# Optimization experiments

Hardware: AMD Instinct MI355X
Metric: run time of the kernel (lower is better)

The kernel has to match this reference:

```python
import jax, jax.numpy as jnp
import numpy as np

# Mamba2 hyperparameters
D_MODEL = 768
D_STATE = 64
D_CONV = 4
EXPAND = 2
HEADDIM = 64
CHUNK = 64
D_INNER = EXPAND * D_MODEL            # 1536
NHEADS = D_INNER // HEADDIM           # 24
D_IN_PROJ = 2 * D_INNER + 2 * D_STATE + NHEADS  # 3224
CONV_DIM = D_INNER + 2 * D_STATE      # 1664
B_SZ = 8
SEQ = 4096  # multiple of CHUNK -> no padding branch


def setup_inputs() -> dict:
    key = jax.random.key(0)
    ks = jax.random.split(key, 6)
    u = jax.random.normal(ks[0], (B_SZ, SEQ, D_MODEL), jnp.float32)
    # fan-in scaled weights (matches nn.Linear/Conv1d default init scale)
    W_in = jax.random.normal(ks[1], (D_IN_PROJ, D_MODEL), jnp.float32) / np.sqrt(D_MODEL).astype(np.float32)
    conv_w = jax.random.normal(ks[2], (CONV_DIM, 1, D_CONV), jnp.float32) / np.sqrt(D_CONV).astype(np.float32)
    conv_b = jnp.zeros((CONV_DIM,), jnp.float32)
    dt_bias = jax.random.uniform(ks[3], (NHEADS,), jnp.float32, -4.0, 1.0)  # nn.init.uniform_(-4, 1)
    A_log = jnp.full((NHEADS,), -np.log(2.0), jnp.float32)                  # nn.init.constant_(-log 2)
    D_param = jnp.ones((NHEADS,), jnp.float32)
    norm_w = jnp.ones((D_INNER,), jnp.float32)
    W_out = jax.random.normal(ks[4], (D_MODEL, D_INNER), jnp.float32) / np.sqrt(D_INNER).astype(np.float32)
    return dict(u=u, W_in=W_in, conv_w=conv_w, conv_b=conv_b, dt_bias=dt_bias,
                A_log=A_log, D_param=D_param, norm_w=norm_w, W_out=W_out)


def _segsum(x):
    """Stable segment sum: out[..., i, j] = sum_{j < k <= i} x[..., k]; -inf above diagonal."""
    T = x.shape[-1]
    lower_strict = jnp.tril(jnp.ones((T, T), bool), -1)
    xe = jnp.where(lower_strict, x[..., :, None], 0.0)   # broadcast x over last (col) axis
    s = jnp.cumsum(xe, axis=-2)
    lower = jnp.tril(jnp.ones((T, T), bool), 0)
    return jnp.where(lower, s, -jnp.inf)


def _ssd(x, A, B, C, chunk):
    """Chunked SSD. x:(b,L,h,p)  A:(b,L,h)  B,C:(b,L,1,n)."""
    b, L, h, p = x.shape
    c = L // chunk
    n = B.shape[-1]
    x = x.reshape(b, c, chunk, h, p)
    A = A.reshape(b, c, chunk, h).transpose(0, 3, 1, 2)   # b h c l
    B = B.reshape(b, c, chunk, 1, n)
    C = C.reshape(b, c, chunk, 1, n)
    A_cs = jnp.cumsum(A, axis=-1)                          # b h c l
    # intra-chunk (diagonal) term
    Lmat = jnp.exp(_segsum(A))                             # b h c l s
    Y_diag = jnp.einsum('bclhn,bcshn,bhcls,bcshp->bclhp', C, B, Lmat, x)
    # per-chunk states
    decay_states = jnp.exp(A_cs[..., -1:] - A_cs)          # b h c l
    states = jnp.einsum('bclhn,bhcl,bclhp->bchpn', B, decay_states, x)
    states = jnp.concatenate([jnp.zeros_like(states[:, :1]), states], axis=1)  # b (c+1) h p n
    # inter-chunk recurrence
    A_last = jnp.pad(A_cs[..., -1], ((0, 0), (0, 0), (1, 0)))  # b h (c+1)
    decay_chunk = jnp.exp(_segsum(A_last))                     # b h (c+1) (c+1)
    new_states = jnp.einsum('bhzc,bchpn->bzhpn', decay_chunk, states)
    states = new_states[:, :-1]                                # b c h p n
    # off-diagonal (state-to-output) term
    Y_off = jnp.einsum('bclhn,bchpn,bhcl->bclhp', C, states, jnp.exp(A_cs))
    return (Y_diag + Y_off).reshape(b, L, h, p)


def reference(u, W_in, conv_w, conv_b, dt_bias, A_log, D_param, norm_w, W_out):
    b, L, _ = u.shape  # L % CHUNK == 0, so pad branch is a no-op
    zxbcdt = u @ W_in.T                                    # (b, L, D_IN_PROJ)
    z = zxbcdt[..., :D_INNER]
    xBC = zxbcdt[..., D_INNER:D_INNER + CONV_DIM]
    dt = jax.nn.softplus(zxbcdt[..., D_INNER + CONV_DIM:] + dt_bias)  # (b, L, h)
    # causal depthwise conv1d (torch pads both sides by d_conv-1 then slices [:L] == left pad)
    xBC = jax.lax.conv_general_dilated(
        xBC.transpose(0, 2, 1), conv_w, window_strides=(1,),
        padding=[(D_CONV - 1, 0)], dimension_numbers=('NCH', 'OIH', 'NCH'),
        feature_group_count=CONV_DIM)
    xBC = jax.nn.silu(xBC.transpose(0, 2, 1) + conv_b)     # (b, L, CONV_DIM)
    x = xBC[..., :D_INNER].reshape(b, L, NHEADS, HEADDIM)
    Bm = xBC[..., D_INNER:D_INNER + D_STATE][:, :, None, :]  # (b, L, 1, n)
    Cm = xBC[..., D_INNER + D_STATE:][:, :, None, :]
    A = -jnp.exp(A_log)                                    # (h,)
    Y = _ssd(x * dt[..., None], A * dt, Bm, Cm, CHUNK)
    y = Y + x * D_param[:, None]                           # skip term
    y = y.reshape(b, L, D_INNER)
    # gated RMSNorm: x * silu(z), then rmsnorm * weight
    y = y * jax.nn.silu(z)
    y = y * jax.lax.rsqrt(jnp.mean(y * y, axis=-1, keepdims=True) + 1e-5) * norm_w
    return y @ W_out.T
```

## Files before the change

kernel.cpp:

```cpp
#include <hip/hip_runtime.h>
#include <stdint.h>

typedef unsigned short u16;
typedef __bf16 bf16x8 __attribute__((ext_vector_type(8)));
typedef float f32x4 __attribute__((ext_vector_type(4)));
typedef unsigned short u16x8 __attribute__((ext_vector_type(8)));
typedef unsigned short u16x4 __attribute__((ext_vector_type(4)));
typedef __attribute__((address_space(1))) unsigned int gu32;
typedef __attribute__((address_space(3))) unsigned int lu32;

__device__ __forceinline__ float bf2f(u16 u){ unsigned int v=((unsigned int)u)<<16; float f; __builtin_memcpy(&f,&v,4); return f; }
__device__ __forceinline__ u16 f2bf(float f){ unsigned int v; __builtin_memcpy(&v,&f,4); v += 0x7fffu + ((v>>16)&1u); return (u16)(v>>16); }
__device__ __forceinline__ int swz(int r,int c){ return (r<<6) + (c ^ ((r&7)<<3)); }
__device__ __forceinline__ void glds16(const void* g, void* l){
  __builtin_amdgcn_global_load_lds((gu32*)g, (lu32*)l, 16, 0, 0);
}

__global__ __launch_bounds__(256) void k_cast(const float* __restrict__ in, u16* __restrict__ out, int n4){
  int i = blockIdx.x*256 + threadIdx.x;
  if (i >= n4) return;
  const f32x4 v = *(const f32x4*)(in + (size_t)i*4);
  u16x4 o; o.x=f2bf(v.x); o.y=f2bf(v.y); o.z=f2bf(v.z); o.w=f2bf(v.w);
  *(u16x4*)(out + (size_t)i*4) = o;
}

__global__ __launch_bounds__(256) void k_cast_pad(const float* __restrict__ in, u16* __restrict__ out){
  int i = blockIdx.x*256 + threadIdx.x;
  int e0 = i*4;
  int row = e0 / 768;
  int col = e0 - row*768;
  u16x4 o;
  if (row < 3224){
    const f32x4 v = *(const f32x4*)(in + (size_t)row*768 + col);
    o.x=f2bf(v.x); o.y=f2bf(v.y); o.z=f2bf(v.z); o.w=f2bf(v.w);
  } else { o.x=0; o.y=0; o.z=0; o.w=0; }
  *(u16x4*)(out + e0) = o;
}

template<int K, int NT, int EPI>
__global__ __launch_bounds__(256,4) void k_gemm(
    const u16* __restrict__ A, const u16* __restrict__ Bw,
    u16* __restrict__ o_z, u16* __restrict__ o_xbc, float* __restrict__ o_dt,
    const float* __restrict__ dt_bias, float* __restrict__ o_f32)
{
  __shared__ __align__(16) u16 Alds[8192];
  __shared__ __align__(16) u16 Blds[8192];
  const int tid = threadIdx.x;
  const int wave = tid>>6, lane = tid&63;
  const int nwg = gridDim.x;
  const int cpx = nwg>>3;
  const int bid = (int)blockIdx.x;
  const int sb  = (bid&7)*cpx + (bid>>3);
  const int m0 = (sb/NT)<<7, n0 = (sb%NT)<<7;
  const int wr = (wave>>1)<<6, wc = (wave&1)<<6;
  const int srow = tid>>3, sc0 = (tid&7)<<3;
  const int lo16 = lane&15, hi = lane>>4;
  f32x4 acc[4][4] = {};
  for (int k0 = 0; k0 < K; k0 += 64){
    #pragma unroll
    for (int i = 0; i < 4; ++i){
      const int row = (i<<5) + srow;
      const int scol = sc0 ^ ((row&7)<<3);
      glds16(A  + (size_t)(m0+row)*K + k0 + scol, &Alds[(i<<11) + (wave<<9)]);
      glds16(Bw + (size_t)(n0+row)*K + k0 + scol, &Blds[(i<<11) + (wave<<9)]);
    }
    __syncthreads();
    #pragma unroll
    for (int kk = 0; kk < 2; ++kk){
      const int kb = (kk<<5) + (hi<<3);
      bf16x8 af[4], bfv[4];
      #pragma unroll
      for (int m = 0; m < 4; ++m){
        const int r = wr + (m<<4) + lo16;
        af[m] = *(const bf16x8*)&Alds[(r<<6) + (kb ^ ((r&7)<<3))];
      }
      #pragma unroll
      for (int n = 0; n < 4; ++n){
        const int r = wc + (n<<4) + lo16;
        bfv[n] = *(const bf16x8*)&Blds[(r<<6) + (kb ^ ((r&7)<<3))];
      }
      #pragma unroll
      for (int m = 0; m < 4; ++m)
      #pragma unroll
      for (int n = 0; n < 4; ++n)
        acc[m][n] = __builtin_amdgcn_mfma_f32_16x16x32_bf16(af[m], bfv[n], acc[m][n], 0,0,0);
    }
    __syncthreads();
  }
  #pragma unroll
  for (int m = 0; m < 4; ++m)
  #pragma unroll
  for (int n = 0; n < 4; ++n)
  #pragma unroll
  for (int i = 0; i < 4; ++i){
    const int gr = m0 + wr + (m<<4) + (hi<<2) + i;
    const int gc = n0 + wc + (n<<4) + lo16;
    const float v = acc[m][n][i];
    if constexpr (EPI == 0){
      if (gc < 1536)      o_z[(size_t)gr*1536 + gc] = f2bf(v);
      else if (gc < 3200) o_xbc[(size_t)gr*1664 + (gc-1536)] = f2bf(v);
      else if (gc < 3224){
        const float t = v + dt_bias[gc-3200];
        o_dt[(size_t)(gc-3200)*32768 + gr] = (t > 20.f) ? t : log1pf(__expf(t));
      }
    } else {
      o_f32[(size_t)gr*768 + gc] = v;
    }
  }
}

__global__ __launch_bounds__(256) void k_conv(
    const u16* __restrict__ xbc, const float* __restrict__ cw, const float* __restrict__ cb,
    const float* __restrict__ dtT,
    u16* __restrict__ xT, u16* __restrict__ Bn, u16* __restrict__ BT, u16* __restrict__ Cn)
{
  const int idx = blockIdx.x*256 + threadIdx.x;
  if (idx >= 4096*208) return;
  const int g  = idx % 208;
  const int pt = idx / 208;
  const int ch0 = g << 3;
  const int m0 = pt << 3;
  const int l0 = m0 & 4095;
  float wgt[8][4], bias8[8];
  #pragma unroll
  for (int j = 0; j < 8; ++j){
    const f32x4 wv = *(const f32x4*)(cw + (size_t)(ch0+j)*4);
    wgt[j][0]=wv.x; wgt[j][1]=wv.y; wgt[j][2]=wv.z; wgt[j][3]=wv.w;
    bias8[j] = cb[ch0+j];
  }
  float acc[8][8];
  #pragma unroll
  for (int p = 0; p < 8; ++p)
  #pragma unroll
  for (int j = 0; j < 8; ++j) acc[p][j] = bias8[j];
  #pragma unroll
  for (int r = -3; r < 8; ++r){
    const int ls = l0 + r;
    if (ls < 0) continue;
    const u16x8 v = *(const u16x8*)(xbc + (size_t)(m0+r)*1664 + ch0);
    float xf[8];
    #pragma unroll
    for (int j = 0; j < 8; ++j) xf[j] = bf2f(v[j]);
    #pragma unroll
    for (int t = 0; t < 4; ++t){
      const int p = r + 3 - t;
      if (p < 0 || p > 7) continue;
      #pragma unroll
      for (int j = 0; j < 8; ++j) acc[p][j] += xf[j] * wgt[j][t];
    }
  }
  #pragma unroll
  for (int p = 0; p < 8; ++p)
  #pragma unroll
  for (int j = 0; j < 8; ++j){ const float s = acc[p][j]; acc[p][j] = s / (1.f + __expf(-s)); }

  const int b = m0 >> 12;
  const int cch = l0 >> 6;
  const int lr0 = l0 & 63;
  if (ch0 < 1536){
    const int h = ch0 >> 6, p0 = ch0 & 63;
    const f32x4 d0 = *(const f32x4*)(dtT + (size_t)h*32768 + m0);
    const f32x4 d1 = *(const f32x4*)(dtT + (size_t)h*32768 + m0 + 4);
    const float dtl[8] = {d0.x,d0.y,d0.z,d0.w,d1.x,d1.y,d1.z,d1.w};
    const size_t rb = (size_t)(b*24+h)*64;
    #pragma unroll
    for (int j = 0; j < 8; ++j){
      const int row = p0 + j;
      u16x8 o;
      #pragma unroll
      for (int p = 0; p < 8; ++p) o[p] = f2bf(acc[p][j] * dtl[p]);
      *(u16x8*)(xT + (rb + row)*4096 + (size_t)cch*64 + (lr0 ^ ((row&7)<<3))) = o;
    }
  } else if (ch0 < 1600){
    const int n0 = ch0 - 1536;
    const size_t tb = ((size_t)(b*64 + cch))*4096;
    #pragma unroll
    for (int p = 0; p < 8; ++p){
      const int lr = lr0 + p;
      u16x8 o;
      #pragma unroll
      for (int j = 0; j < 8; ++j) o[j] = f2bf(acc[p][j]);
      *(u16x8*)(Bn + tb + lr*64 + (n0 ^ ((lr&7)<<3))) = o;
    }
    #pragma unroll
    for (int j = 0; j < 8; ++j){
      const int row = n0 + j;
      u16x8 o;
      #pragma unroll
      for (int p = 0; p < 8; ++p) o[p] = f2bf(acc[p][j]);
      *(u16x8*)(BT + tb + row*64 + (lr0 ^ ((row&7)<<3))) = o;
    }
  } else {
    const int n0 = ch0 - 1600;
    const size_t tb = ((size_t)(b*64 + cch))*4096;
    #pragma unroll
    for (int p = 0; p < 8; ++p){
      const int lr = lr0 + p;
      u16x8 o;
      #pragma unroll
      for (int j = 0; j < 8; ++j) o[j] = f2bf(acc[p][j]);
      *(u16x8*)(Cn + tb + lr*64 + (n0 ^ ((lr&7)<<3))) = o;
    }
  }
}

__global__ __launch_bounds__(256,2) void k_ssd(
    const u16* __restrict__ xT, const u16* __restrict__ Bn, const u16* __restrict__ BT,
    const u16* __restrict__ Cn, const float* __restrict__ dtT, const float* __restrict__ A_log,
    const float* __restrict__ Dp, u16* __restrict__ yo)
{
  __shared__ __align__(16) u16 Xq[2][1024];
  __shared__ __align__(16) u16 Bnl[2][4096];
  __shared__ __align__(16) u16 BTl[2][4096];
  __shared__ __align__(16) u16 Cnl[2][4096];
  __shared__ __align__(16) u16 Ml[4096];
  __shared__ __align__(16) u16 Sbf[1024];
  const int tid = threadIdx.x, wave = tid>>6, lane = tid&63;
  const int lo16 = lane&15, hi = lane>>4;
  const int w16 = wave<<4, hi4 = hi<<2;
  const int bid = (int)blockIdx.x;
  const int b = bid / 96, rem = bid % 96, h = rem >> 2, p0 = (rem&3) << 4;
  const float Ah = -__expf(A_log[h]);
  const float Dh = Dp[h];
  for (int i = tid; i < 1024; i += 256) Sbf[i] = 0;
  f32x4 Sreg = {};
  const size_t xTg  = (size_t)(b*24+h)*64*4096;
  const size_t bcg  = (size_t)b*64*4096;
  const size_t dtg0 = (size_t)h*32768 + (size_t)b*4096;
  const size_t yb   = (size_t)b*4096*1536 + (size_t)h*64;

  auto stage = [&](int buf, int c){
    if (wave == 0){
      const u16* g0 = xT + xTg + (size_t)c*64 + (size_t)(p0 + (lane>>3))*4096 + (lane&7)*8;
      glds16(g0,               &Xq[buf][0]);
      glds16(g0 + 8*4096,      &Xq[buf][512]);
    } else {
      const u16* src = (wave==1 ? Bn : wave==2 ? BT : Cn) + bcg + (size_t)c*4096 + lane*8;
      u16* dst = (wave==1 ? &Bnl[buf][0] : wave==2 ? &BTl[buf][0] : &Cnl[buf][0]);
      #pragma unroll
      for (int s = 0; s < 8; ++s) glds16(src + s*512, dst + s*512);
    }
  };

  float dtc = dtT[dtg0 + lane];
  stage(0, 0);

  for (int c = 0; c < 64; ++c){
    float s = Ah * dtc;
    #pragma unroll
    for (int o = 1; o < 64; o <<= 1){ const float t = __shfl_up(s, o); if (lane >= o) s += t; }
    const float Alast = __shfl(s, 63);
    const float lam  = __expf(Alast);
    const float decl = __expf(Alast - s);
    const float elv  = __expf(s);
    float dtn = 0.f;
    if (c < 63){
      dtn = dtT[dtg0 + (size_t)(c+1)*64 + lane];
      stage((c+1)&1, c+1);
    }
    if (c == 0){
      if (wave == 0) asm volatile("s_waitcnt vmcnt(2) lgkmcnt(0)" ::: "memory");
      else           asm volatile("s_waitcnt vmcnt(8) lgkmcnt(0)" ::: "memory");
    } else if (c == 63){
      asm volatile("s_waitcnt vmcnt(0) lgkmcnt(0)" ::: "memory");
    } else {
      if (wave == 0) asm volatile("s_waitcnt vmcnt(3) lgkmcnt(0)" ::: "memory");
      else           asm volatile("s_waitcnt vmcnt(9) lgkmcnt(0)" ::: "memory");
    }
    __builtin_amdgcn_s_barrier();

    const u16* tx = &Xq[c&1][0];
    const u16* tb = &Bnl[c&1][0];
    const u16* tt = &BTl[c&1][0];
    const u16* tc = &Cnl[c&1][0];

    f32x4 accG[4] = {};
    #pragma unroll
    for (int kk = 0; kk < 2; ++kk){
      const int kb = (kk<<5) + (hi<<3);
      const int rA = w16 + lo16;
      const bf16x8 aB = *(const bf16x8*)&tb[(rA<<6) + (kb ^ ((rA&7)<<3))];
      #pragma unroll
      for (int t = 0; t < 4; ++t){
        const int rb = (t<<4) + lo16;
        const bf16x8 bfC = *(const bf16x8*)&tc[(rb<<6) + (kb ^ ((rb&7)<<3))];
        accG[t] = __builtin_amdgcn_mfma_f32_16x16x32_bf16(aB, bfC, accG[t], 0,0,0);
      }
    }
    float As_i[4];
    #pragma unroll
    for (int i = 0; i < 4; ++i) As_i[i] = __shfl(s, w16 + hi4 + i);
    #pragma unroll
    for (int t = 0; t < 4; ++t){
      const int l = (t<<4) + lo16;
      const float Al  = __shfl(s, l);
      const float dtl = __shfl(dtc, l);
      u16x4 ov;
      #pragma unroll
      for (int i = 0; i < 4; ++i){
        const int si = w16 + hi4 + i;
        float v = 0.f;
        if (si <= l) v = accG[t][i] * __expf(Al - As_i[i]);
        if (si == l) v += Dh / dtl;
        ov[i] = f2bf(v);
      }
      *(u16x4*)&Ml[(l<<6) + ((w16 + hi4) ^ ((l&7)<<3))] = ov;
    }
    asm volatile("s_waitcnt lgkmcnt(0)" ::: "memory");
    __builtin_amdgcn_s_barrier();

    f32x4 aYd = {}, aYo = {}, aS = {};
    #pragma unroll
    for (int kk = 0; kk < 2; ++kk){
      const int kb = (kk<<5) + (hi<<3);
      const int oP = (lo16<<6) + (kb ^ ((lo16&7)<<3));
      const int rW = w16 + lo16;
      const int oW = (rW<<6) + (kb ^ ((rW&7)<<3));
      const bf16x8 aX  = *(const bf16x8*)&tx[oP];
      const bf16x8 aSb = *(const bf16x8*)&Sbf[oP];
      const u16x8 aBTu = *(const u16x8*)&tt[oW];
      u16x8 aBTs;
      #pragma unroll
      for (int j = 0; j < 8; ++j) aBTs[j] = f2bf(bf2f(aBTu[j]) * __shfl(decl, kb + j));
      const bf16x8 aBT = *(const bf16x8*)&aBTs;
      const bf16x8 bM  = *(const bf16x8*)&Ml[oW];
      const bf16x8 bC  = *(const bf16x8*)&tc[oW];
      aYd = __builtin_amdgcn_mfma_f32_16x16x32_bf16(aX,  bM, aYd, 0,0,0);
      aYo = __builtin_amdgcn_mfma_f32_16x16x32_bf16(aSb, bC, aYo, 0,0,0);
      aS  = __builtin_amdgcn_mfma_f32_16x16x32_bf16(aBT, aX, aS,  0,0,0);
    }
    asm volatile("s_waitcnt lgkmcnt(0)" ::: "memory");
    __builtin_amdgcn_s_barrier();

    {
      u16x4 sv;
      #pragma unroll
      for (int i = 0; i < 4; ++i){
        const float nv = Sreg[i] * lam + aS[i];
        Sreg[i] = nv;
        sv[i] = f2bf(nv);
      }
      *(u16x4*)&Sbf[(lo16<<6) + ((w16 + hi4) ^ ((lo16&7)<<3))] = sv;
    }
    {
      const int l = w16 + lo16;
      const float elt = __shfl(elv, l);
      u16x4 ov;
      #pragma unroll
      for (int i = 0; i < 4; ++i) ov[i] = f2bf(aYd[i] + elt * aYo[i]);
      *(u16x4*)(yo + yb + (size_t)((c<<6)+l)*1536 + p0 + hi4) = ov;
    }
    dtc = dtn;
  }
}

__global__ __launch_bounds__(192) void k_gnorm(
    const u16* __restrict__ y, const u16* __restrict__ z,
    const float* __restrict__ nw, u16* __restrict__ out)
{
  __shared__ float red[3];
  const int m = blockIdx.x, t = threadIdx.x;
  const size_t base = (size_t)m*1536 + t*8;
  const u16x8 yv = *(const u16x8*)(y + base);
  const u16x8 zv = *(const u16x8*)(z + base);
  float vals[8]; float ss = 0.f;
  #pragma unroll
  for (int j = 0; j < 8; ++j){
    const float zf = bf2f(zv[j]);
    const float v = bf2f(yv[j]) * zf / (1.f + __expf(-zf));
    vals[j] = v; ss += v*v;
  }
  #pragma unroll
  for (int off = 32; off > 0; off >>= 1) ss += __shfl_down(ss, off);
  if ((t & 63) == 0) red[t>>6] = ss;
  __syncthreads();
  const float sc = rsqrtf((red[0]+red[1]+red[2]) * (1.f/1536.f) + 1e-5f);
  u16x8 o;
  #pragma unroll
  for (int j = 0; j < 8; ++j) o[j] = f2bf(vals[j] * sc * nw[t*8+j]);
  *(u16x8*)(out + base) = o;
}

extern "C" void kernel_launch(void* const* d_in, const int* in_sizes, int n_in,
                              void* d_out, int out_size, void* d_ws, size_t ws_size,
                              hipStream_t stream)
{
  const float* u       = (const float*)d_in[0];
  const float* W_in    = (const float*)d_in[1];
  const float* conv_w  = (const float*)d_in[2];
  const float* conv_b  = (const float*)d_in[3];
  const float* dt_bias = (const float*)d_in[4];
  const float* A_log   = (const float*)d_in[5];
  const float* D_param = (const float*)d_in[6];
  const float* norm_w  = (const float*)d_in[7];
  const float* W_out   = (const float*)d_in[8];
  (void)in_sizes; (void)n_in; (void)out_size;
  if (ws_size < (size_t)379715584) return;

  char* w = (char*)d_ws;
  size_t off = 0;
  auto alloc = [&](size_t bytes)->void*{ void* p = w + off; off += (bytes + 255) & ~(size_t)255; return p; };
  u16* ubf    = (u16*)alloc(50331648);
  u16* winbf  = (u16*)alloc(5111808);
  u16* woutbf = (u16*)alloc(2359296);
  u16* zbf    = (u16*)alloc(100663296);
  u16* xbcbf  = (u16*)alloc(109051904);
  float* dtT  = (float*)alloc(3145728);
  u16* xTb    = (u16*)alloc(100663296);
  u16* Bnb    = (u16*)alloc(4194304);
  u16* Cnb    = (u16*)alloc(4194304);
  u16* BTb    = ubf;
  u16* yssd   = xbcbf;
  u16* ynorm  = xTb;

  k_cast<<<24576, 256, 0, stream>>>(u, ubf, 6291456);
  k_cast_pad<<<2496, 256, 0, stream>>>(W_in, winbf);
  k_cast<<<1152, 256, 0, stream>>>(W_out, woutbf, 294912);
  k_gemm<768,26,0><<<6656, 256, 0, stream>>>(ubf, winbf, zbf, xbcbf, dtT, dt_bias, nullptr);
  k_conv<<<3328, 256, 0, stream>>>(xbcbf, conv_w, conv_b, dtT, xTb, Bnb, BTb, Cnb);
  k_ssd<<<768, 256, 0, stream>>>(xTb, Bnb, BTb, Cnb, dtT, A_log, D_param, yssd);
  k_gnorm<<<32768, 192, 0, stream>>>(yssd, zbf, norm_w, ynorm);
  k_gemm<1536,6,1><<<1536, 256, 0, stream>>>(ynorm, woutbf, nullptr, nullptr, nullptr, nullptr, (float*)d_out);
}
```

Baseline: 796.3 us.

## Widen SSD blocks to 32 head-dim columns and remap GEMM tile order

The SSD kernel now runs 512 threads per block covering 32 head-dim columns, so the B/C/BT chunk tiles loaded into LDS are shared across twice as many columns and the per-chunk B·C mask work is split over 8 waves. A double-buffered state tile lets the block drop one barrier per chunk. The GEMM block-to-tile mapping is also changed to an XCD-aware grouping in N passes to improve L2 reuse. The cost is larger LDS use per block, which may limit occupancy, and hand-tuned vmcnt waits that must match the new load counts.

```diff
diff --git a/kernel.cpp b/kernel.cpp
--- a/kernel.cpp
+++ b/kernel.cpp
@@ -11,7 +11,6 @@
 
 __device__ __forceinline__ float bf2f(u16 u){ unsigned int v=((unsigned int)u)<<16; float f; __builtin_memcpy(&f,&v,4); return f; }
 __device__ __forceinline__ u16 f2bf(float f){ unsigned int v; __builtin_memcpy(&v,&f,4); v += 0x7fffu + ((v>>16)&1u); return (u16)(v>>16); }
-__device__ __forceinline__ int swz(int r,int c){ return (r<<6) + (c ^ ((r&7)<<3)); }
 __device__ __forceinline__ void glds16(const void* g, void* l){
   __builtin_amdgcn_global_load_lds((gu32*)g, (lu32*)l, 16, 0, 0);
 }
@@ -37,7 +36,7 @@
   *(u16x4*)(out + e0) = o;
 }
 
-template<int K, int NT, int EPI>
+template<int K, int NT, int NH, int EPI>
 __global__ __launch_bounds__(256,4) void k_gemm(
     const u16* __restrict__ A, const u16* __restrict__ Bw,
     u16* __restrict__ o_z, u16* __restrict__ o_xbc, float* __restrict__ o_dt,
@@ -47,11 +46,14 @@
   __shared__ __align__(16) u16 Blds[8192];
   const int tid = threadIdx.x;
   const int wave = tid>>6, lane = tid&63;
-  const int nwg = gridDim.x;
-  const int cpx = nwg>>3;
+  constexpr int NPH = NT / NH;
   const int bid = (int)blockIdx.x;
-  const int sb  = (bid&7)*cpx + (bid>>3);
-  const int m0 = (sb/NT)<<7, n0 = (sb%NT)<<7;
+  const int x = bid & 7;
+  const int q = bid >> 3;
+  const int pass = q / (32*NPH);
+  const int rem  = q % (32*NPH);
+  const int m0 = ((x<<5) + rem/NPH) << 7;
+  const int n0 = (pass*NPH + rem%NPH) << 7;
   const int wr = (wave>>1)<<6, wc = (wave&1)<<6;
   const int srow = tid>>3, sc0 = (tid&7)<<3;
   const int lo16 = lane&15, hi = lane>>4;
@@ -204,25 +206,26 @@
   }
 }
 
-__global__ __launch_bounds__(256,2) void k_ssd(
+__global__ __launch_bounds__(512,4) void k_ssd(
     const u16* __restrict__ xT, const u16* __restrict__ Bn, const u16* __restrict__ BT,
     const u16* __restrict__ Cn, const float* __restrict__ dtT, const float* __restrict__ A_log,
     const float* __restrict__ Dp, u16* __restrict__ yo)
 {
-  __shared__ __align__(16) u16 Xq[2][1024];
+  __shared__ __align__(16) u16 Xq[2][2048];
   __shared__ __align__(16) u16 Bnl[2][4096];
   __shared__ __align__(16) u16 BTl[2][4096];
   __shared__ __align__(16) u16 Cnl[2][4096];
   __shared__ __align__(16) u16 Ml[4096];
-  __shared__ __align__(16) u16 Sbf[1024];
+  __shared__ __align__(16) u16 Sbf[2][2048];
   const int tid = threadIdx.x, wave = tid>>6, lane = tid&63;
+  const int pA = wave>>2, lB = wave&3;
   const int lo16 = lane&15, hi = lane>>4;
-  const int w16 = wave<<4, hi4 = hi<<2;
+  const int hi4 = hi<<2;
   const int bid = (int)blockIdx.x;
-  const int b = bid / 96, rem = bid % 96, h = rem >> 2, p0 = (rem&3) << 4;
+  const int b = bid / 48, rem = bid % 48, h = rem>>1, ph = rem&1;
   const float Ah = -__expf(A_log[h]);
   const float Dh = Dp[h];
-  for (int i = tid; i < 1024; i += 256) Sbf[i] = 0;
+  for (int i = tid; i < 4096; i += 512) ((u16*)Sbf)[i] = 0;
   f32x4 Sreg = {};
   const size_t xTg  = (size_t)(b*24+h)*64*4096;
   const size_t bcg  = (size_t)b*64*4096;
@@ -231,14 +234,20 @@
 
   auto stage = [&](int buf, int c){
     if (wave == 0){
-      const u16* g0 = xT + xTg + (size_t)c*64 + (size_t)(p0 + (lane>>3))*4096 + (lane&7)*8;
-      glds16(g0,               &Xq[buf][0]);
-      glds16(g0 + 8*4096,      &Xq[buf][512]);
-    } else {
-      const u16* src = (wave==1 ? Bn : wave==2 ? BT : Cn) + bcg + (size_t)c*4096 + lane*8;
-      u16* dst = (wave==1 ? &Bnl[buf][0] : wave==2 ? &BTl[buf][0] : &Cnl[buf][0]);
-      #pragma unroll
-      for (int s = 0; s < 8; ++s) glds16(src + s*512, dst + s*512);
+      const u16* g0 = xT + xTg + (size_t)c*64 + (size_t)(ph*32 + (lane>>3))*4096 + (lane&7)*8;
+      u16* dst = &Xq[buf][0];
+      #pragma unroll
+      for (int s = 0; s < 4; ++s) glds16(g0 + (size_t)s*8*4096, dst + s*512);
+    } else if (wave < 7){
+      const int kind = (wave-1)>>1;
+      const int hb = (wave-1)&1;
+      const u16* src = (kind==0 ? Bn : kind==1 ? BT : Cn) + bcg + (size_t)c*4096 + lane*8;
+      u16* dst = (kind==0 ? &Bnl[buf][0] : kind==1 ? &BTl[buf][0] : &Cnl[buf][0]);
+      #pragma unroll
+      for (int s = 0; s < 4; ++s){
+        const int sx = hb*4 + s;
+        glds16(src + sx*512, dst + sx*512);
+      }
     }
   };
 
@@ -258,80 +267,71 @@
       dtn = dtT[dtg0 + (size_t)(c+1)*64 + lane];
       stage((c+1)&1, c+1);
     }
-    if (c == 0){
-      if (wave == 0) asm volatile("s_waitcnt vmcnt(2) lgkmcnt(0)" ::: "memory");
-      else           asm volatile("s_waitcnt vmcnt(8) lgkmcnt(0)" ::: "memory");
-    } else if (c == 63){
-      asm volatile("s_waitcnt vmcnt(0) lgkmcnt(0)" ::: "memory");
-    } else {
-      if (wave == 0) asm volatile("s_waitcnt vmcnt(3) lgkmcnt(0)" ::: "memory");
-      else           asm volatile("s_waitcnt vmcnt(9) lgkmcnt(0)" ::: "memory");
-    }
+    if (c == 0)       asm volatile("s_waitcnt vmcnt(5) lgkmcnt(0)" ::: "memory");
+    else if (c == 63) asm volatile("s_waitcnt vmcnt(1) lgkmcnt(0)" ::: "memory");
+    else              asm volatile("s_waitcnt vmcnt(6) lgkmcnt(0)" ::: "memory");
     __builtin_amdgcn_s_barrier();
 
-    const u16* tx = &Xq[c&1][0];
-    const u16* tb = &Bnl[c&1][0];
-    const u16* tt = &BTl[c&1][0];
-    const u16* tc = &Cnl[c&1][0];
-
-    f32x4 accG[4] = {};
+    const int cb = c&1;
+    const u16* Sr = &Sbf[cb][0];
+    u16*       Sw = &Sbf[cb^1][0];
+
+    const int sRow = (lB<<4) + lo16;
+    f32x4 accG[2] = {};
     #pragma unroll
     for (int kk = 0; kk < 2; ++kk){
       const int kb = (kk<<5) + (hi<<3);
-      const int rA = w16 + lo16;
-      const bf16x8 aB = *(const bf16x8*)&tb[(rA<<6) + (kb ^ ((rA&7)<<3))];
-      #pragma unroll
-      for (int t = 0; t < 4; ++t){
-        const int rb = (t<<4) + lo16;
-        const bf16x8 bfC = *(const bf16x8*)&tc[(rb<<6) + (kb ^ ((rb&7)<<3))];
-        accG[t] = __builtin_amdgcn_mfma_f32_16x16x32_bf16(aB, bfC, accG[t], 0,0,0);
+      const bf16x8 aB = *(const bf16x8*)&Bnl[cb][(sRow<<6) + (kb ^ ((sRow&7)<<3))];
+      #pragma unroll
+      for (int g = 0; g < 2; ++g){
+        const int lr = (((pA<<1)+g)<<4) + lo16;
+        const bf16x8 bC1 = *(const bf16x8*)&Cnl[cb][(lr<<6) + (kb ^ ((lr&7)<<3))];
+        accG[g] = __builtin_amdgcn_mfma_f32_16x16x32_bf16(aB, bC1, accG[g], 0,0,0);
       }
     }
     float As_i[4];
     #pragma unroll
-    for (int i = 0; i < 4; ++i) As_i[i] = __shfl(s, w16 + hi4 + i);
-    #pragma unroll
-    for (int t = 0; t < 4; ++t){
-      const int l = (t<<4) + lo16;
+    for (int i = 0; i < 4; ++i) As_i[i] = __shfl(s, (lB<<4) + hi4 + i);
+    #pragma unroll
+    for (int g = 0; g < 2; ++g){
+      const int l = (((pA<<1)+g)<<4) + lo16;
       const float Al  = __shfl(s, l);
       const float dtl = __shfl(dtc, l);
       u16x4 ov;
       #pragma unroll
       for (int i = 0; i < 4; ++i){
-        const int si = w16 + hi4 + i;
+        const int si = (lB<<4) + hi4 + i;
         float v = 0.f;
-        if (si <= l) v = accG[t][i] * __expf(Al - As_i[i]);
+        if (si <= l) v = accG[g][i] * __expf(Al - As_i[i]);
         if (si == l) v += Dh / dtl;
         ov[i] = f2bf(v);
       }
-      *(u16x4*)&Ml[(l<<6) + ((w16 + hi4) ^ ((l&7)<<3))] = ov;
+      *(u16x4*)&Ml[(l<<6) + (((lB<<4) + hi4) ^ ((l&7)<<3))] = ov;
     }
     asm volatile("s_waitcnt lgkmcnt(0)" ::: "memory");
     __builtin_amdgcn_s_barrier();
 
+    const int pRow = (pA<<4) + lo16;
+    const int lRow = (lB<<4) + lo16;
     f32x4 aYd = {}, aYo = {}, aS = {};
     #pragma unroll
     for (int kk = 0; kk < 2; ++kk){
       const int kb = (kk<<5) + (hi<<3);
-      const int oP = (lo16<<6) + (kb ^ ((lo16&7)<<3));
-      const int rW = w16 + lo16;
-      const int oW = (rW<<6) + (kb ^ ((rW&7)<<3));
-      const bf16x8 aX  = *(const bf16x8*)&tx[oP];
-      const bf16x8 aSb = *(const bf16x8*)&Sbf[oP];
-      const u16x8 aBTu = *(const u16x8*)&tt[oW];
+      const int oP = (pRow<<6) + (kb ^ ((pRow&7)<<3));
+      const int oL = (lRow<<6) + (kb ^ ((lRow&7)<<3));
+      const bf16x8 aX  = *(const bf16x8*)&Xq[cb][oP];
+      const bf16x8 aSb = *(const bf16x8*)&Sr[oP];
+      const u16x8 aBTu = *(const u16x8*)&BTl[cb][oL];
       u16x8 aBTs;
       #pragma unroll
       for (int j = 0; j < 8; ++j) aBTs[j] = f2bf(bf2f(aBTu[j]) * __shfl(decl, kb + j));
       const bf16x8 aBT = *(const bf16x8*)&aBTs;
-      const bf16x8 bM  = *(const bf16x8*)&Ml[oW];
-      const bf16x8 bC  = *(const bf16x8*)&tc[oW];
+      const bf16x8 bM  = *(const bf16x8*)&Ml[oL];
+      const bf16x8 bC  = *(const bf16x8*)&Cnl[cb][oL];
       aYd = __builtin_amdgcn_mfma_f32_16x16x32_bf16(aX,  bM, aYd, 0,0,0);
       aYo = __builtin_amdgcn_mfma_f32_16x16x32_bf16(aSb, bC, aYo, 0,0,0);
       aS  = __builtin_amdgcn_mfma_f32_16x16x32_bf16(aBT, aX, aS,  0,0,0);
     }
-    asm volatile("s_waitcnt lgkmcnt(0)" ::: "memory");
-    __builtin_amdgcn_s_barrier();
-
     {
       u16x4 sv;
       #pragma unroll
@@ -340,15 +340,14 @@
         Sreg[i] = nv;
         sv[i] = f2bf(nv);
       }
-      *(u16x4*)&Sbf[(lo16<<6) + ((w16 + hi4) ^ ((lo16&7)<<3))] = sv;
+      *(u16x4*)&Sw[(pRow<<6) + ((((lB<<4) + hi4)) ^ ((pRow&7)<<3))] = sv;
     }
     {
-      const int l = w16 + lo16;
-      const float elt = __shfl(elv, l);
+      const float elt = __shfl(elv, lRow);
       u16x4 ov;
       #pragma unroll
       for (int i = 0; i < 4; ++i) ov[i] = f2bf(aYd[i] + elt * aYo[i]);
-      *(u16x4*)(yo + yb + (size_t)((c<<6)+l)*1536 + p0 + hi4) = ov;
+      *(u16x4*)(yo + yb + (size_t)((c<<6)+lRow)*1536 + ph*32 + (pA<<4) + hi4) = ov;
     }
     dtc = dtn;
   }
@@ -416,9 +415,9 @@
   k_cast<<<24576, 256, 0, stream>>>(u, ubf, 6291456);
   k_cast_pad<<<2496, 256, 0, stream>>>(W_in, winbf);
   k_cast<<<1152, 256, 0, stream>>>(W_out, woutbf, 294912);
-  k_gemm<768,26,0><<<6656, 256, 0, stream>>>(ubf, winbf, zbf, xbcbf, dtT, dt_bias, nullptr);
+  k_gemm<768,26,2,0><<<6656, 256, 0, stream>>>(ubf, winbf, zbf, xbcbf, dtT, dt_bias, nullptr);
   k_conv<<<3328, 256, 0, stream>>>(xbcbf, conv_w, conv_b, dtT, xTb, Bnb, BTb, Cnb);
-  k_ssd<<<768, 256, 0, stream>>>(xTb, Bnb, BTb, Cnb, dtT, A_log, D_param, yssd);
+  k_ssd<<<384, 512, 0, stream>>>(xTb, Bnb, BTb, Cnb, dtT, A_log, D_param, yssd);
   k_gnorm<<<32768, 192, 0, stream>>>(yssd, zbf, norm_w, ynorm);
-  k_gemm<1536,6,1><<<1536, 256, 0, stream>>>(ynorm, woutbf, nullptr, nullptr, nullptr, nullptr, (float*)d_out);
-}
+  k_gemm<1536,6,1,1><<<1536, 256, 0, stream>>>(ynorm, woutbf, nullptr, nullptr, nullptr, nullptr, (float*)d_out);
+}
```

After: 705.0 us. 11.5% less time.
